# Kernel tuning notes

Hardware: AMD Instinct MI355X
Metric: run time of the kernel (lower is better)

## Reference

```python
import jax, jax.numpy as jnp
import numpy as np

B, T, D_MODEL, D_HIDDEN, MAX_SEQLEN = 4, 2048, 1024, 1024, 2048


def setup_inputs() -> dict:
    key = jax.random.key(0)
    ks = jax.random.split(key, 8)
    scale = 0.02  # keep exp() and linear outputs in a sane range
    return {
        "q": jax.random.normal(ks[0], (B, T, D_MODEL), dtype=jnp.float32),
        "k": jax.random.normal(ks[1], (B, T, D_MODEL), dtype=jnp.float32),
        "v": jax.random.normal(ks[2], (B, T, D_MODEL), dtype=jnp.float32),
        "Wq": jax.random.normal(ks[3], (D_HIDDEN, D_MODEL), dtype=jnp.float32) * scale,
        "Wk": jax.random.normal(ks[4], (D_HIDDEN, D_MODEL), dtype=jnp.float32) * scale,
        "Wv": jax.random.normal(ks[5], (D_HIDDEN, D_MODEL), dtype=jnp.float32) * scale,
        "Wo": jax.random.normal(ks[6], (D_MODEL, D_HIDDEN), dtype=jnp.float32) * scale,
        "W_bias": jax.random.normal(ks[7], (MAX_SEQLEN, MAX_SEQLEN), dtype=jnp.float32) * scale,
    }


def reference(q, k, v, Wq, Wk, Wv, Wo, W_bias):
    Ti = q.shape[1]
    Tj = k.shape[1]
    # Linear projections (torch Linear: x @ W.T), bias=False
    Q = jnp.einsum('btm,hm->bth', q, Wq)
    K = jnp.einsum('btm,hm->bth', k, Wk)
    V = jnp.einsum('btm,hm->bth', v, Wv)
    pos_bias = W_bias[:Ti, :Tj][None]              # (1, Ti, Tj)
    # Faithful to original: max over dim 0 (batch dim for K, singleton dim for pos_bias)
    max_key = jnp.max(K, axis=0, keepdims=True)    # (1, Tj, Dh)
    max_pos_bias = jnp.max(pos_bias, axis=0, keepdims=True)  # == pos_bias (dim 0 is size 1)
    exp_key = jnp.exp(K - max_key)                 # (B, Tj, Dh)
    exp_pos_bias = jnp.exp(pos_bias - max_pos_bias)  # all-ones, kept for faithfulness
    num = jnp.einsum('bij,bjd->bid', exp_pos_bias, exp_key * V)
    den = jnp.einsum('bij,bjd->bid', exp_pos_bias, exp_key)
    Yt = jax.nn.sigmoid(Q) * num / den             # (B, Ti, Dh)
    return jnp.einsum('bth,mh->btm', Yt, Wo)
```

## Files before the change

kernel.cpp:

```cpp
#include <hip/hip_runtime.h>
#include <hip/hip_bf16.h>

typedef __bf16 bf16;
typedef __bf16 bf16x8 __attribute__((ext_vector_type(8)));
typedef __bf16 bf16x4 __attribute__((ext_vector_type(4)));
typedef float f32x4 __attribute__((ext_vector_type(4)));

#define B_   4
#define T_   2048
#define DM_  1024
#define DH_  1024
#define MROWS (B_ * T_)

struct CvtJob { const float* src; bf16* dst; int n; };
struct CvtArgs { CvtJob job[7]; };

__global__ __launch_bounds__(256) void cvt_kernel(CvtArgs args) {
  CvtJob jb = args.job[blockIdx.y];
  int i = (blockIdx.x * 256 + threadIdx.x) * 8;
  if (i >= jb.n) return;
  const float4* s = (const float4*)(jb.src + i);
  float4 a = s[0];
  float4 b = s[1];
  bf16x8 o;
  o[0] = (bf16)a.x; o[1] = (bf16)a.y; o[2] = (bf16)a.z; o[3] = (bf16)a.w;
  o[4] = (bf16)b.x; o[5] = (bf16)b.y; o[6] = (bf16)b.z; o[7] = (bf16)b.w;
  *(bf16x8*)(jb.dst + i) = o;
}

__global__ __launch_bounds__(256) void gemm_bt(
    const bf16* __restrict__ A, const bf16* __restrict__ B,
    float* __restrict__ C, int M, int N, int K) {
  __shared__ bf16 As[128 * 64];
  __shared__ bf16 Bs[128 * 64];

  const int tid  = threadIdx.x;
  const int lane = tid & 63;
  const int wave = tid >> 6;
  const int wm   = (wave >> 1) * 64;
  const int wn   = (wave & 1) * 64;
  const int tileM = blockIdx.y * 128;
  const int tileN = blockIdx.x * 128;

  f32x4 acc[4][4] = {};

  const int sr = lane >> 3;
  const int sc = (lane & 7) ^ sr;

  for (int k0 = 0; k0 < K; k0 += 64) {
#pragma unroll
    for (int l = 0; l < 4; ++l) {
      int grp = wave * 4 + l;
      int row = grp * 8 + sr;
      const bf16* ga = A + (size_t)(tileM + row) * K + k0 + sc * 8;
      __builtin_amdgcn_global_load_lds(
          (const __attribute__((address_space(1))) void*)ga,
          (__attribute__((address_space(3))) void*)&As[grp * 512], 16, 0, 0);
      const bf16* gb = B + (size_t)(tileN + row) * K + k0 + sc * 8;
      __builtin_amdgcn_global_load_lds(
          (const __attribute__((address_space(1))) void*)gb,
          (__attribute__((address_space(3))) void*)&Bs[grp * 512], 16, 0, 0);
    }
    __syncthreads();

    const int quad = lane >> 4;
#pragma unroll
    for (int s = 0; s < 2; ++s) {
      bf16x8 af[4], bfr[4];
#pragma unroll
      for (int mt = 0; mt < 4; ++mt) {
        int row = wm + mt * 16 + (lane & 15);
        int chunk = (s * 4 + quad) ^ (row & 7);
        af[mt] = *(const bf16x8*)&As[row * 64 + chunk * 8];
      }
#pragma unroll
      for (int nt = 0; nt < 4; ++nt) {
        int row = wn + nt * 16 + (lane & 15);
        int chunk = (s * 4 + quad) ^ (row & 7);
        bfr[nt] = *(const bf16x8*)&Bs[row * 64 + chunk * 8];
      }
#pragma unroll
      for (int mt = 0; mt < 4; ++mt)
#pragma unroll
        for (int nt = 0; nt < 4; ++nt)
          acc[mt][nt] = __builtin_amdgcn_mfma_f32_16x16x32_bf16(
              af[mt], bfr[nt], acc[mt][nt], 0, 0, 0);
    }
    __syncthreads();
  }

  const int cn = lane & 15;
  const int cr = (lane >> 4) * 4;
#pragma unroll
  for (int mt = 0; mt < 4; ++mt)
#pragma unroll
    for (int nt = 0; nt < 4; ++nt)
#pragma unroll
      for (int r = 0; r < 4; ++r) {
        int row = tileM + wm + mt * 16 + cr + r;
        int col = tileN + wn + nt * 16 + cn;
        C[(size_t)row * N + col] = acc[mt][nt][r];
      }
}

__global__ __launch_bounds__(256) void reduce_kv(
    const float* __restrict__ Kf, const float* __restrict__ Vf,
    float* __restrict__ num, float* __restrict__ den) {
  const int d  = blockIdx.x * 256 + threadIdx.x;
  const int j0 = blockIdx.y * 32;
  const size_t bs = (size_t)T_ * DH_;
  float n0 = 0, n1 = 0, n2 = 0, n3 = 0, e0 = 0, e1 = 0, e2 = 0, e3 = 0;
#pragma unroll 2
  for (int j = j0; j < j0 + 32; ++j) {
    size_t off = (size_t)j * DH_ + d;
    float k0 = Kf[off], k1 = Kf[off + bs], k2 = Kf[off + 2 * bs], k3 = Kf[off + 3 * bs];
    float v0 = Vf[off], v1 = Vf[off + bs], v2 = Vf[off + 2 * bs], v3 = Vf[off + 3 * bs];
    float m = fmaxf(fmaxf(k0, k1), fmaxf(k2, k3));
    float w0 = __expf(k0 - m), w1 = __expf(k1 - m);
    float w2 = __expf(k2 - m), w3 = __expf(k3 - m);
    e0 += w0; e1 += w1; e2 += w2; e3 += w3;
    n0 += w0 * v0; n1 += w1 * v1; n2 += w2 * v2; n3 += w3 * v3;
  }
  atomicAdd(&num[0 * DH_ + d], n0);
  atomicAdd(&num[1 * DH_ + d], n1);
  atomicAdd(&num[2 * DH_ + d], n2);
  atomicAdd(&num[3 * DH_ + d], n3);
  atomicAdd(&den[0 * DH_ + d], e0);
  atomicAdd(&den[1 * DH_ + d], e1);
  atomicAdd(&den[2 * DH_ + d], e2);
  atomicAdd(&den[3 * DH_ + d], e3);
}

__global__ __launch_bounds__(256) void make_y(
    const float* __restrict__ Qf, const float* __restrict__ num,
    const float* __restrict__ den, bf16* __restrict__ Yb) {
  size_t i = ((size_t)blockIdx.x * 256 + threadIdx.x) * 4;
  int h = (int)(i & (DH_ - 1));
  int b = (int)(i >> 21);
  float4 qv = *(const float4*)(Qf + i);
  float r0 = num[b * DH_ + h + 0] / den[b * DH_ + h + 0];
  float r1 = num[b * DH_ + h + 1] / den[b * DH_ + h + 1];
  float r2 = num[b * DH_ + h + 2] / den[b * DH_ + h + 2];
  float r3 = num[b * DH_ + h + 3] / den[b * DH_ + h + 3];
  bf16x4 y;
  y[0] = (bf16)(r0 / (1.f + __expf(-qv.x)));
  y[1] = (bf16)(r1 / (1.f + __expf(-qv.y)));
  y[2] = (bf16)(r2 / (1.f + __expf(-qv.z)));
  y[3] = (bf16)(r3 / (1.f + __expf(-qv.w)));
  *(bf16x4*)(Yb + i) = y;
}

extern "C" void kernel_launch(void* const* d_in, const int* in_sizes, int n_in,
                              void* d_out, int out_size, void* d_ws, size_t ws_size,
                              hipStream_t stream) {
  const float* q  = (const float*)d_in[0];
  const float* k  = (const float*)d_in[1];
  const float* v  = (const float*)d_in[2];
  const float* Wq = (const float*)d_in[3];
  const float* Wk = (const float*)d_in[4];
  const float* Wv = (const float*)d_in[5];
  const float* Wo = (const float*)d_in[6];
  float* out = (float*)d_out;

  char* ws = (char*)d_ws;
  size_t off = 0;
  auto alloc = [&](size_t bytes) {
    char* p = ws + off;
    off += (bytes + 255) & ~(size_t)255;
    return p;
  };
  const size_t actN = (size_t)MROWS * DM_;
  const size_t wN   = (size_t)DH_ * DM_;

  bf16* qb  = (bf16*)alloc(actN * 2);
  bf16* kb  = (bf16*)alloc(actN * 2);
  bf16* vb  = (bf16*)alloc(actN * 2);
  bf16* Wqb = (bf16*)alloc(wN * 2);
  bf16* Wkb = (bf16*)alloc(wN * 2);
  bf16* Wvb = (bf16*)alloc(wN * 2);
  bf16* Wob = (bf16*)alloc(wN * 2);
  float* Qf = (float*)alloc(actN * 4);
  float* Kf = (float*)alloc(actN * 4);
  float* Vf = (float*)alloc(actN * 4);
  float* num = (float*)alloc(B_ * DH_ * 4);
  float* den = (float*)alloc(B_ * DH_ * 4);
  bf16* Yb = qb;

  CvtArgs ca;
  ca.job[0] = {q,  qb,  (int)actN};
  ca.job[1] = {k,  kb,  (int)actN};
  ca.job[2] = {v,  vb,  (int)actN};
  ca.job[3] = {Wq, Wqb, (int)wN};
  ca.job[4] = {Wk, Wkb, (int)wN};
  ca.job[5] = {Wv, Wvb, (int)wN};
  ca.job[6] = {Wo, Wob, (int)wN};
  cvt_kernel<<<dim3(actN / 8 / 256, 7), 256, 0, stream>>>(ca);

  dim3 ggrid(DH_ / 128, MROWS / 128);

  gemm_bt<<<ggrid, 256, 0, stream>>>(kb, Wkb, Kf, MROWS, DH_, DM_);
  gemm_bt<<<ggrid, 256, 0, stream>>>(vb, Wvb, Vf, MROWS, DH_, DM_);
  gemm_bt<<<ggrid, 256, 0, stream>>>(qb, Wqb, Qf, MROWS, DH_, DM_);

  hipMemsetAsync(num, 0, 2 * B_ * DH_ * sizeof(float), stream);
  reduce_kv<<<dim3(4, 64), 256, 0, stream>>>(Kf, Vf, num, den);

  make_y<<<dim3(actN / 4 / 256), 256, 0, stream>>>(Qf, num, den, Yb);

  gemm_bt<<<ggrid, 256, 0, stream>>>(Yb, Wob, out, MROWS, DM_, DH_);
}
```

Baseline: 294.7 us.

## Batch projection GEMMs, fuse sigmoid into Q epilogue, fold num/den into Wo

The three projection GEMMs now run as a single launch with a z-dimension job index. The Q GEMM epilogue writes sigmoid(Q) directly as bf16, which removes the fp32 Q buffer and the make_y pass. The per-batch num/den ratio is folded into a per-batch scaled copy of Wo, and the output GEMM runs as four batched jobs. The convert kernel also processes more elements per thread. This removes a full activation-sized read and write pass and several launches, at the cost of four bf16 Wo copies and an extra rounding of the num/den scale into the weights.

After: 290.8 us. No clear change (-1.3%).

```diff
diff --git a/kernel.cpp b/kernel.cpp
--- a/kernel.cpp
+++ b/kernel.cpp
@@ -12,25 +12,33 @@
 #define DH_  1024
 #define MROWS (B_ * T_)
 
-struct CvtJob { const float* src; bf16* dst; int n; };
-struct CvtArgs { CvtJob job[7]; };
+struct CvtJob { const float* src; bf16* dst; int nf4; };
+struct CvtArgs { CvtJob job[6]; };
 
 __global__ __launch_bounds__(256) void cvt_kernel(CvtArgs args) {
   CvtJob jb = args.job[blockIdx.y];
-  int i = (blockIdx.x * 256 + threadIdx.x) * 8;
-  if (i >= jb.n) return;
-  const float4* s = (const float4*)(jb.src + i);
-  float4 a = s[0];
-  float4 b = s[1];
-  bf16x8 o;
-  o[0] = (bf16)a.x; o[1] = (bf16)a.y; o[2] = (bf16)a.z; o[3] = (bf16)a.w;
-  o[4] = (bf16)b.x; o[5] = (bf16)b.y; o[6] = (bf16)b.z; o[7] = (bf16)b.w;
-  *(bf16x8*)(jb.dst + i) = o;
-}
-
-__global__ __launch_bounds__(256) void gemm_bt(
-    const bf16* __restrict__ A, const bf16* __restrict__ B,
-    float* __restrict__ C, int M, int N, int K) {
+  int f4 = blockIdx.x * 1024 + threadIdx.x * 2;
+  if (f4 >= jb.nf4) return;
+  const float4* s = (const float4*)jb.src;
+  float4 a0 = s[f4];
+  float4 a1 = s[f4 + 1];
+  float4 b0 = s[f4 + 512];
+  float4 b1 = s[f4 + 513];
+  bf16x8 oa, ob;
+  oa[0] = (bf16)a0.x; oa[1] = (bf16)a0.y; oa[2] = (bf16)a0.z; oa[3] = (bf16)a0.w;
+  oa[4] = (bf16)a1.x; oa[5] = (bf16)a1.y; oa[6] = (bf16)a1.z; oa[7] = (bf16)a1.w;
+  ob[0] = (bf16)b0.x; ob[1] = (bf16)b0.y; ob[2] = (bf16)b0.z; ob[3] = (bf16)b0.w;
+  ob[4] = (bf16)b1.x; ob[5] = (bf16)b1.y; ob[6] = (bf16)b1.z; ob[7] = (bf16)b1.w;
+  *(bf16x8*)(jb.dst + (size_t)f4 * 4) = oa;
+  *(bf16x8*)(jb.dst + (size_t)(f4 + 512) * 4) = ob;
+}
+
+struct GemmJob { const bf16* A; const bf16* Bw; float* Cf; bf16* Cb; };
+struct GemmArgs { GemmJob job[4]; int N; int K; };
+
+__global__ __launch_bounds__(256) void gemm_bt(GemmArgs ga) {
+  const GemmJob jb = ga.job[blockIdx.z];
+  const int N = ga.N, K = ga.K;
   __shared__ bf16 As[128 * 64];
   __shared__ bf16 Bs[128 * 64];
 
@@ -52,13 +60,13 @@
     for (int l = 0; l < 4; ++l) {
       int grp = wave * 4 + l;
       int row = grp * 8 + sr;
-      const bf16* ga = A + (size_t)(tileM + row) * K + k0 + sc * 8;
+      const bf16* gaadr = jb.A + (size_t)(tileM + row) * K + k0 + sc * 8;
       __builtin_amdgcn_global_load_lds(
-          (const __attribute__((address_space(1))) void*)ga,
+          (const __attribute__((address_space(1))) void*)gaadr,
           (__attribute__((address_space(3))) void*)&As[grp * 512], 16, 0, 0);
-      const bf16* gb = B + (size_t)(tileN + row) * K + k0 + sc * 8;
+      const bf16* gbadr = jb.Bw + (size_t)(tileN + row) * K + k0 + sc * 8;
       __builtin_amdgcn_global_load_lds(
-          (const __attribute__((address_space(1))) void*)gb,
+          (const __attribute__((address_space(1))) void*)gbadr,
           (__attribute__((address_space(3))) void*)&Bs[grp * 512], 16, 0, 0);
     }
     __syncthreads();
@@ -91,16 +99,30 @@
 
   const int cn = lane & 15;
   const int cr = (lane >> 4) * 4;
-#pragma unroll
-  for (int mt = 0; mt < 4; ++mt)
-#pragma unroll
-    for (int nt = 0; nt < 4; ++nt)
-#pragma unroll
-      for (int r = 0; r < 4; ++r) {
-        int row = tileM + wm + mt * 16 + cr + r;
-        int col = tileN + wn + nt * 16 + cn;
-        C[(size_t)row * N + col] = acc[mt][nt][r];
-      }
+  if (jb.Cf) {
+#pragma unroll
+    for (int mt = 0; mt < 4; ++mt)
+#pragma unroll
+      for (int nt = 0; nt < 4; ++nt)
+#pragma unroll
+        for (int r = 0; r < 4; ++r) {
+          int row = tileM + wm + mt * 16 + cr + r;
+          int col = tileN + wn + nt * 16 + cn;
+          jb.Cf[(size_t)row * N + col] = acc[mt][nt][r];
+        }
+  } else {
+#pragma unroll
+    for (int mt = 0; mt < 4; ++mt)
+#pragma unroll
+      for (int nt = 0; nt < 4; ++nt)
+#pragma unroll
+        for (int r = 0; r < 4; ++r) {
+          int row = tileM + wm + mt * 16 + cr + r;
+          int col = tileN + wn + nt * 16 + cn;
+          float sv = 1.f / (1.f + __expf(-acc[mt][nt][r]));
+          jb.Cb[(size_t)row * N + col] = (bf16)sv;
+        }
+  }
 }
 
 __global__ __launch_bounds__(256) void reduce_kv(
@@ -131,23 +153,23 @@
   atomicAdd(&den[3 * DH_ + d], e3);
 }
 
-__global__ __launch_bounds__(256) void make_y(
-    const float* __restrict__ Qf, const float* __restrict__ num,
-    const float* __restrict__ den, bf16* __restrict__ Yb) {
-  size_t i = ((size_t)blockIdx.x * 256 + threadIdx.x) * 4;
-  int h = (int)(i & (DH_ - 1));
-  int b = (int)(i >> 21);
-  float4 qv = *(const float4*)(Qf + i);
-  float r0 = num[b * DH_ + h + 0] / den[b * DH_ + h + 0];
-  float r1 = num[b * DH_ + h + 1] / den[b * DH_ + h + 1];
-  float r2 = num[b * DH_ + h + 2] / den[b * DH_ + h + 2];
-  float r3 = num[b * DH_ + h + 3] / den[b * DH_ + h + 3];
-  bf16x4 y;
-  y[0] = (bf16)(r0 / (1.f + __expf(-qv.x)));
-  y[1] = (bf16)(r1 / (1.f + __expf(-qv.y)));
-  y[2] = (bf16)(r2 / (1.f + __expf(-qv.z)));
-  y[3] = (bf16)(r3 / (1.f + __expf(-qv.w)));
-  *(bf16x4*)(Yb + i) = y;
+__global__ __launch_bounds__(256) void scale_wo(
+    const float* __restrict__ Wo, const float* __restrict__ num,
+    const float* __restrict__ den, bf16* __restrict__ Wos) {
+  int i = (blockIdx.x * 256 + threadIdx.x) * 4;
+  int h = i & (DH_ - 1);
+  float4 w = *(const float4*)(Wo + i);
+#pragma unroll
+  for (int b = 0; b < 4; ++b) {
+    float4 nu = *(const float4*)(num + b * DH_ + h);
+    float4 de = *(const float4*)(den + b * DH_ + h);
+    bf16x4 o;
+    o[0] = (bf16)(w.x * nu.x / de.x);
+    o[1] = (bf16)(w.y * nu.y / de.y);
+    o[2] = (bf16)(w.z * nu.z / de.z);
+    o[3] = (bf16)(w.w * nu.w / de.w);
+    *(bf16x4*)(Wos + (size_t)b * DH_ * DM_ + i) = o;
+  }
 }
 
 extern "C" void kernel_launch(void* const* d_in, const int* in_sizes, int n_in,
@@ -178,34 +200,40 @@
   bf16* Wqb = (bf16*)alloc(wN * 2);
   bf16* Wkb = (bf16*)alloc(wN * 2);
   bf16* Wvb = (bf16*)alloc(wN * 2);
-  bf16* Wob = (bf16*)alloc(wN * 2);
-  float* Qf = (float*)alloc(actN * 4);
   float* Kf = (float*)alloc(actN * 4);
   float* Vf = (float*)alloc(actN * 4);
+  bf16* Yb  = (bf16*)alloc(actN * 2);
+  bf16* Wos = (bf16*)alloc(4 * wN * 2);
   float* num = (float*)alloc(B_ * DH_ * 4);
   float* den = (float*)alloc(B_ * DH_ * 4);
-  bf16* Yb = qb;
 
   CvtArgs ca;
-  ca.job[0] = {q,  qb,  (int)actN};
-  ca.job[1] = {k,  kb,  (int)actN};
-  ca.job[2] = {v,  vb,  (int)actN};
-  ca.job[3] = {Wq, Wqb, (int)wN};
-  ca.job[4] = {Wk, Wkb, (int)wN};
-  ca.job[5] = {Wv, Wvb, (int)wN};
-  ca.job[6] = {Wo, Wob, (int)wN};
-  cvt_kernel<<<dim3(actN / 8 / 256, 7), 256, 0, stream>>>(ca);
-
-  dim3 ggrid(DH_ / 128, MROWS / 128);
-
-  gemm_bt<<<ggrid, 256, 0, stream>>>(kb, Wkb, Kf, MROWS, DH_, DM_);
-  gemm_bt<<<ggrid, 256, 0, stream>>>(vb, Wvb, Vf, MROWS, DH_, DM_);
-  gemm_bt<<<ggrid, 256, 0, stream>>>(qb, Wqb, Qf, MROWS, DH_, DM_);
+  ca.job[0] = {q,  qb,  (int)(actN / 4)};
+  ca.job[1] = {k,  kb,  (int)(actN / 4)};
+  ca.job[2] = {v,  vb,  (int)(actN / 4)};
+  ca.job[3] = {Wq, Wqb, (int)(wN / 4)};
+  ca.job[4] = {Wk, Wkb, (int)(wN / 4)};
+  ca.job[5] = {Wv, Wvb, (int)(wN / 4)};
+  cvt_kernel<<<dim3(actN / 4 / 1024, 6), 256, 0, stream>>>(ca);
 
   hipMemsetAsync(num, 0, 2 * B_ * DH_ * sizeof(float), stream);
+
+  GemmArgs g1;
+  g1.N = DH_; g1.K = DM_;
+  g1.job[0] = {kb, Wkb, Kf, nullptr};
+  g1.job[1] = {vb, Wvb, Vf, nullptr};
+  g1.job[2] = {qb, Wqb, nullptr, Yb};
+  g1.job[3] = {nullptr, nullptr, nullptr, nullptr};
+  gemm_bt<<<dim3(DH_ / 128, MROWS / 128, 3), 256, 0, stream>>>(g1);
+
   reduce_kv<<<dim3(4, 64), 256, 0, stream>>>(Kf, Vf, num, den);
 
-  make_y<<<dim3(actN / 4 / 256), 256, 0, stream>>>(Qf, num, den, Yb);
-
-  gemm_bt<<<ggrid, 256, 0, stream>>>(Yb, Wob, out, MROWS, DM_, DH_);
-}
+  scale_wo<<<dim3(wN / 4 / 256), 256, 0, stream>>>(Wo, num, den, Wos);
+
+  GemmArgs g2;
+  g2.N = DM_; g2.K = DH_;
+  for (int b = 0; b < 4; ++b)
+    g2.job[b] = {Yb + (size_t)b * T_ * DH_, Wos + (size_t)b * wN,
+                 out + (size_t)b * T_ * DM_, nullptr};
+  gemm_bt<<<dim3(DM_ / 128, T_ / 128, 4), 256, 0, stream>>>(g2);
+}
```
